# Kernel optimization log

Measured on AMD Instinct MI355X. Metric: run time of the kernel, lower is better.

The kernel has to match this reference:

```python
import jax, jax.numpy as jnp
import numpy as np

D_MODEL = 768
N_HEADS = 4
D_HEAD = D_MODEL // N_HEADS
EPS = 1e-3  # keras LayerNormalization default


def gelu_tanh(x):
    return 0.5 * x * (1.0 + jnp.tanh(np.sqrt(2.0 / np.pi) * (x + 0.044715 * x ** 3)))


def layer_norm(x, g, b):
    mu = jnp.mean(x, axis=-1, keepdims=True)
    var = jnp.mean(jnp.square(x - mu), axis=-1, keepdims=True)
    return (x - mu) * jax.lax.rsqrt(var + EPS) * g + b


def setup_inputs() -> dict:
    key = jax.random.key(0)
    ks = jax.random.split(key, 12)
    B, S = 8, 1024
    x = jax.random.normal(ks[0], (B, S, D_MODEL), dtype=jnp.float32)
    # causal mask: 1 on strictly-future positions (added as mask * -1e9)
    mask = jnp.triu(jnp.ones((S, S), dtype=jnp.float32), k=1)[None, None]
    s = 0.02
    params = {
        'W1': jax.random.normal(ks[1], (D_MODEL, 3 * D_MODEL)) * s,
        'b1': jnp.zeros((3 * D_MODEL,), jnp.float32),
        'W3': jax.random.normal(ks[2], (D_MODEL, D_MODEL)) * s,
        'b3': jnp.zeros((D_MODEL,), jnp.float32),
        'W2': jax.random.normal(ks[3], (D_MODEL, 4 * D_MODEL)) * s,
        'b2': jnp.zeros((4 * D_MODEL,), jnp.float32),
        'W4': jax.random.normal(ks[4], (4 * D_MODEL, D_MODEL)) * s,
        'b4': jnp.zeros((D_MODEL,), jnp.float32),
        'g1': jnp.ones((D_MODEL,), jnp.float32),
        'be1': jnp.zeros((D_MODEL,), jnp.float32),
        'g2': jnp.ones((D_MODEL,), jnp.float32),
        'be2': jnp.zeros((D_MODEL,), jnp.float32),
    }
    return {'x': x, 'mask': mask, **params}


def reference(x, mask, W1, b1, W3, b3, W2, b2, W4, b4, g1, be1, g2, be2):
    B, S, _ = x.shape
    xn = layer_norm(x, g1, be1)
    qkv = xn @ W1 + b1                                  # [B,S,3D]
    q, k, v = jnp.split(qkv, 3, axis=-1)
    def split_heads(t):
        return t.reshape(B, S, N_HEADS, D_HEAD).transpose(0, 2, 1, 3)  # [B,H,S,dh]
    q, k, v = map(split_heads, (q, k, v))
    present = jnp.stack([k, v], axis=1)                  # [B,2,H,S,dh]
    w = jnp.einsum('bhqd,bhkd->bhqk', q, k)
    # NOTE: source divides by rsqrt(d_head) => multiplies by sqrt(d_head) (faithful bug)
    w = w * jnp.sqrt(jnp.float32(D_HEAD))
    w = w + mask * -1e9
    w = jax.nn.softmax(w, axis=-1)
    attn = jnp.einsum('bhqk,bhkd->bhqd', w, v)           # [B,H,S,dh]
    attn = attn.transpose(0, 2, 1, 3).reshape(B, S, D_MODEL)
    x = attn @ W3 + b3 + x                               # residual 1
    xn2 = layer_norm(x, g2, be2)
    h = gelu_tanh(xn2 @ W2 + b2)                         # [B,S,4D]
    x = h @ W4 + b4 + x                                  # residual 2
    return x, present
```

## Files before the change

kernel.cpp:

```cpp
#include <hip/hip_runtime.h>
#include <hip/hip_bf16.h>
#include <cstdint>

#define D_MODEL 768
#define NH 4
#define DH 192
#define SEQ 1024
#define BATCH 8

typedef __bf16 bf16x8 __attribute__((ext_vector_type(8)));
typedef float floatx4 __attribute__((ext_vector_type(4)));

__device__ __forceinline__ float bf2f(ushort u) {
    union { uint32_t i; float f; } x; x.i = ((uint32_t)u) << 16; return x.f;
}
__device__ __forceinline__ ushort f2bf(float f) {
    union { float f; uint32_t i; } x; x.f = f;
    uint32_t i = x.i;
    uint32_t r = (i + 0x7FFFu + ((i >> 16) & 1u)) >> 16;
    return (ushort)r;
}

template <int SPLIT>
__global__ void ln_kernel(const float* __restrict__ x, const float* __restrict__ g,
                          const float* __restrict__ be,
                          ushort* __restrict__ y_hi, ushort* __restrict__ y_lo) {
    int row = blockIdx.x;
    int tid = threadIdx.x;
    const float* xr = x + (size_t)row * D_MODEL;
    float v[3];
    float s = 0.f, ss = 0.f;
#pragma unroll
    for (int i = 0; i < 3; i++) {
        float t = xr[tid + i * 256];
        v[i] = t; s += t; ss += t * t;
    }
#pragma unroll
    for (int off = 32; off > 0; off >>= 1) {
        s += __shfl_down(s, off);
        ss += __shfl_down(ss, off);
    }
    __shared__ float rs[4], rss[4];
    int wid = tid >> 6;
    if ((tid & 63) == 0) { rs[wid] = s; rss[wid] = ss; }
    __syncthreads();
    s = rs[0] + rs[1] + rs[2] + rs[3];
    ss = rss[0] + rss[1] + rss[2] + rss[3];
    float mu = s * (1.f / 768.f);
    float var = ss * (1.f / 768.f) - mu * mu;
    float rstd = rsqrtf(var + 1e-3f);
#pragma unroll
    for (int i = 0; i < 3; i++) {
        int d = tid + i * 256;
        float val = (v[i] - mu) * rstd * g[d] + be[d];
        ushort hi = f2bf(val);
        y_hi[(size_t)row * D_MODEL + d] = hi;
        if (SPLIT) y_lo[(size_t)row * D_MODEL + d] = f2bf(val - bf2f(hi));
    }
}

__global__ void transpose_kernel(const float* __restrict__ W, ushort* __restrict__ Wt,
                                 int K, int N) {
    __shared__ ushort tile[64][65];
    int nt = N >> 6;
    int bk = blockIdx.x / nt, bn = blockIdx.x % nt;
    int tid = threadIdx.x;
#pragma unroll
    for (int i = 0; i < 16; i++) {
        int lin = i * 256 + tid; int r = lin >> 6, c = lin & 63;
        tile[r][c] = f2bf(W[(size_t)(bk * 64 + r) * N + bn * 64 + c]);
    }
    __syncthreads();
#pragma unroll
    for (int i = 0; i < 16; i++) {
        int lin = i * 256 + tid; int r = lin >> 6, c = lin & 63;
        Wt[(size_t)(bn * 64 + r) * K + bk * 64 + c] = tile[c][r];
    }
}

__global__ void transpose_split_kernel(const float* __restrict__ W,
                                       ushort* __restrict__ Wt_hi, ushort* __restrict__ Wt_lo,
                                       int K, int N) {
    __shared__ ushort th[64][65];
    __shared__ ushort tl[64][65];
    int nt = N >> 6;
    int bk = blockIdx.x / nt, bn = blockIdx.x % nt;
    int tid = threadIdx.x;
#pragma unroll
    for (int i = 0; i < 16; i++) {
        int lin = i * 256 + tid; int r = lin >> 6, c = lin & 63;
        float v = W[(size_t)(bk * 64 + r) * N + bn * 64 + c];
        ushort hi = f2bf(v);
        th[r][c] = hi;
        tl[r][c] = f2bf(v - bf2f(hi));
    }
    __syncthreads();
#pragma unroll
    for (int i = 0; i < 16; i++) {
        int lin = i * 256 + tid; int r = lin >> 6, c = lin & 63;
        size_t o = (size_t)(bn * 64 + r) * K + bk * 64 + c;
        Wt_hi[o] = th[c][r];
        Wt_lo[o] = tl[c][r];
    }
}

__global__ void transpose_v_kernel(const float* __restrict__ qkv, ushort* __restrict__ Vtg) {
    __shared__ ushort tile[64][65];
    int bi = blockIdx.x;
    int dt = bi % 12;
    int st = (bi / 12) % 16;
    int b  = bi / 192;
    int tid = threadIdx.x;
#pragma unroll
    for (int i = 0; i < 16; i++) {
        int lin = i * 256 + tid; int r = lin >> 6, c = lin & 63;
        tile[r][c] = f2bf(qkv[(size_t)(b * 1024 + st * 64 + r) * 2304 + 1536 + dt * 64 + c]);
    }
    __syncthreads();
#pragma unroll
    for (int i = 0; i < 16; i++) {
        int lin = i * 256 + tid; int r = lin >> 6, c = lin & 63;
        Vtg[(size_t)(b * 768 + dt * 64 + r) * 1024 + st * 64 + c] = tile[c][r];
    }
}

__global__ __launch_bounds__(256, 2) void gemm_qkv_split(
    const ushort* __restrict__ Ah, const ushort* __restrict__ Al,
    const ushort* __restrict__ Bh, const ushort* __restrict__ Bl,
    const float* __restrict__ bias, float* __restrict__ Cout, int M, int N, int K) {
    __shared__ __align__(16) __bf16 sAh[128][48];
    __shared__ __align__(16) __bf16 sAl[128][48];
    __shared__ __align__(16) __bf16 sBh[128][48];
    __shared__ __align__(16) __bf16 sBl[128][48];
    int tid = threadIdx.x;
    int rowBase = blockIdx.y << 7;
    int colBase = blockIdx.x << 7;
    int wave = tid >> 6, lane = tid & 63;
    int wm = (wave & 1) << 6, wn = (wave >> 1) << 6;
    int lrow = lane & 15, lk = (lane >> 4) << 3;
    floatx4 acc[4][4] = {};

    int lr = tid >> 2;
    int lc = (tid & 3) << 3;
    size_t aoff = (size_t)(rowBase + lr) * K + lc;
    size_t boff = (size_t)(colBase + lr) * K + lc;

    for (int k0 = 0; k0 < K; k0 += 32) {
        uint4 ah0 = *(const uint4*)(Ah + aoff + k0);
        uint4 ah1 = *(const uint4*)(Ah + aoff + (size_t)64 * K + k0);
        uint4 al0 = *(const uint4*)(Al + aoff + k0);
        uint4 al1 = *(const uint4*)(Al + aoff + (size_t)64 * K + k0);
        uint4 bh0 = *(const uint4*)(Bh + boff + k0);
        uint4 bh1 = *(const uint4*)(Bh + boff + (size_t)64 * K + k0);
        uint4 bl0 = *(const uint4*)(Bl + boff + k0);
        uint4 bl1 = *(const uint4*)(Bl + boff + (size_t)64 * K + k0);
        *(uint4*)&sAh[lr][lc] = ah0;  *(uint4*)&sAh[lr + 64][lc] = ah1;
        *(uint4*)&sAl[lr][lc] = al0;  *(uint4*)&sAl[lr + 64][lc] = al1;
        *(uint4*)&sBh[lr][lc] = bh0;  *(uint4*)&sBh[lr + 64][lc] = bh1;
        *(uint4*)&sBl[lr][lc] = bl0;  *(uint4*)&sBl[lr + 64][lc] = bl1;
        __syncthreads();
        bf16x8 afh[4], afl[4], bvh[4], bvl[4];
#pragma unroll
        for (int i = 0; i < 4; i++) {
            afh[i] = *(const bf16x8*)&sAh[wm + i * 16 + lrow][lk];
            afl[i] = *(const bf16x8*)&sAl[wm + i * 16 + lrow][lk];
        }
#pragma unroll
        for (int jj = 0; jj < 4; jj++) {
            bvh[jj] = *(const bf16x8*)&sBh[wn + jj * 16 + lrow][lk];
            bvl[jj] = *(const bf16x8*)&sBl[wn + jj * 16 + lrow][lk];
        }
#pragma unroll
        for (int i = 0; i < 4; i++)
#pragma unroll
            for (int jj = 0; jj < 4; jj++) {
                acc[i][jj] = __builtin_amdgcn_mfma_f32_16x16x32_bf16(afh[i], bvh[jj], acc[i][jj], 0, 0, 0);
                acc[i][jj] = __builtin_amdgcn_mfma_f32_16x16x32_bf16(afh[i], bvl[jj], acc[i][jj], 0, 0, 0);
                acc[i][jj] = __builtin_amdgcn_mfma_f32_16x16x32_bf16(afl[i], bvh[jj], acc[i][jj], 0, 0, 0);
            }
        __syncthreads();
    }
    int cr = (lane >> 4) << 2;
    int cc = lane & 15;
#pragma unroll
    for (int jj = 0; jj < 4; jj++) {
        int col = colBase + wn + jj * 16 + cc;
        float bvs = bias[col];
#pragma unroll
        for (int i = 0; i < 4; i++) {
            int row0 = rowBase + wm + i * 16 + cr;
#pragma unroll
            for (int r = 0; r < 4; r++)
                Cout[(size_t)(row0 + r) * N + col] = acc[i][jj][r] + bvs;
        }
    }
}

template <int GELU, int RES, int OUTF32>
__global__ __launch_bounds__(256, 2) void gemm_bt(
    const ushort* __restrict__ A, const ushort* __restrict__ Bt,
    const float* __restrict__ bias, const float* __restrict__ resid,
    void* __restrict__ Cout, int M, int N, int K) {
    __shared__ __align__(16) __bf16 sA[128][48];
    __shared__ __align__(16) __bf16 sB[128][48];
    int tid = threadIdx.x;
    int rowBase = blockIdx.y << 7;
    int colBase = blockIdx.x << 7;
    int wave = tid >> 6, lane = tid & 63;
    int wm = (wave & 1) << 6, wn = (wave >> 1) << 6;
    int lrow = lane & 15, lk = (lane >> 4) << 3;
    floatx4 acc[4][4] = {};

    int lr = tid >> 2;
    int lc = (tid & 3) << 3;
    const ushort* Ab = A + (size_t)(rowBase + lr) * K + lc;
    const ushort* Bb = Bt + (size_t)(colBase + lr) * K + lc;

    for (int k0 = 0; k0 < K; k0 += 32) {
        uint4 a0 = *(const uint4*)(Ab + k0);
        uint4 a1 = *(const uint4*)(Ab + (size_t)64 * K + k0);
        uint4 b0 = *(const uint4*)(Bb + k0);
        uint4 b1 = *(const uint4*)(Bb + (size_t)64 * K + k0);
        *(uint4*)&sA[lr][lc] = a0;
        *(uint4*)&sA[lr + 64][lc] = a1;
        *(uint4*)&sB[lr][lc] = b0;
        *(uint4*)&sB[lr + 64][lc] = b1;
        __syncthreads();
        bf16x8 af[4], bv[4];
#pragma unroll
        for (int i = 0; i < 4; i++) af[i] = *(const bf16x8*)&sA[wm + i * 16 + lrow][lk];
#pragma unroll
        for (int jj = 0; jj < 4; jj++) bv[jj] = *(const bf16x8*)&sB[wn + jj * 16 + lrow][lk];
#pragma unroll
        for (int i = 0; i < 4; i++)
#pragma unroll
            for (int jj = 0; jj < 4; jj++)
                acc[i][jj] = __builtin_amdgcn_mfma_f32_16x16x32_bf16(af[i], bv[jj], acc[i][jj], 0, 0, 0);
        __syncthreads();
    }
    int cr = (lane >> 4) << 2;
    int cc = lane & 15;
#pragma unroll
    for (int jj = 0; jj < 4; jj++) {
        int col = colBase + wn + jj * 16 + cc;
        float bvs = bias[col];
#pragma unroll
        for (int i = 0; i < 4; i++) {
            int row0 = rowBase + wm + i * 16 + cr;
#pragma unroll
            for (int r = 0; r < 4; r++) {
                int row = row0 + r;
                float v = acc[i][jj][r] + bvs;
                if (GELU) {
                    float u = v;
                    v = 0.5f * u * (1.f + tanhf(0.7978845608028654f * (u + 0.044715f * u * u * u)));
                }
                if (RES) v += resid[(size_t)row * N + col];
                if (OUTF32) ((float*)Cout)[(size_t)row * N + col] = v;
                else ((ushort*)Cout)[(size_t)row * N + col] = f2bf(v);
            }
        }
    }
}

__global__ void split_kernel(const float* __restrict__ qkv, float* __restrict__ present,
                             ushort* __restrict__ Khg, ushort* __restrict__ Klg) {
    int tok = blockIdx.x;
    int tid = threadIdx.x;
    int b = tok >> 10, s = tok & 1023;
    const float* src = qkv + (size_t)tok * 2304 + 768;
#pragma unroll
    for (int i = 0; i < 6; i++) {
        int c = tid + i * 256;
        float v = src[c];
        int kv = (c >= 768) ? 1 : 0;
        int within = c - kv * 768;
        int h = within / DH;
        int d = within - h * DH;
        size_t idx = ((size_t)(((b * 2 + kv) * NH + h) * SEQ + s)) * DH + d;
        present[idx] = v;
        if (!kv) {
            ushort hi = f2bf(v);
            Khg[(size_t)tok * 768 + c] = hi;
            Klg[(size_t)tok * 768 + c] = f2bf(v - bf2f(hi));
        }
    }
}

__global__ __launch_bounds__(512, 2) void attn_flash(
    const float* __restrict__ qkv, const ushort* __restrict__ Khg,
    const ushort* __restrict__ Klg, const ushort* __restrict__ Vtg,
    ushort* __restrict__ attn2) {
    int bi = blockIdx.x;
    int j = bi & 7;
    int h = (bi >> 3) & 3;
    int b = bi >> 5;
    int tid = threadIdx.x;
    int wave = tid >> 6, lane = tid & 63;
    int l15 = lane & 15, quad = lane >> 4;
    int tile = (wave < 4) ? (15 - j) : j;
    int w16 = wave & 3;
    int s0 = tile << 6;
    int its = 2 * (15 - j) + 2;
    int myKt = (s0 + w16 * 16 + 15) >> 5;

    __shared__ __align__(16) __bf16 sKh[2][32][200];
    __shared__ __align__(16) __bf16 sKl[2][32][200];
    __shared__ __align__(16) __bf16 sVt[2][192][40];
    __shared__ __align__(16) ushort sP[8][16][40];

    const bool lo_half = (tid < 256);
    const int kr0 = tid / 24, ke0 = (tid % 24) * 8;
    const int c1 = lo_half ? (512 + tid) : (256 + tid);
    const int kr1 = c1 / 24, ke1 = (c1 % 24) * 8;
    const int vd0 = tid >> 2, ve0 = (tid & 3) * 8;
    const int vd1 = (512 + tid) >> 2, ve1 = ((512 + tid) & 3) * 8;

    const ushort* Khb = Khg + (size_t)(b * 1024) * 768 + h * 192;
    const ushort* Klb = Klg + (size_t)(b * 1024) * 768 + h * 192;
    const ushort* Vtb = Vtg + ((size_t)(b * 768) + h * 192) * 1024;
    const ushort* Bb = lo_half ? Khb : Klb;
    __bf16* pKB = lo_half ? &sKh[0][kr1][ke1] : &sKl[0][kr1][ke1];

    uint4 rA, rB, rC, rD, rE;

    rA = *(const uint4*)(Khb + (size_t)kr0 * 768 + ke0);
    rC = *(const uint4*)(Klb + (size_t)kr0 * 768 + ke0);
    rB = *(const uint4*)(Bb + (size_t)kr1 * 768 + ke1);
    rD = *(const uint4*)(Vtb + (size_t)vd0 * 1024 + ve0);
    if (lo_half) rE = *(const uint4*)(Vtb + (size_t)vd1 * 1024 + ve1);

    bf16x8 qh[6], ql[6];
    {
        int qrow = s0 + w16 * 16 + l15;
        const float* qp = qkv + (size_t)(b * SEQ + qrow) * 2304 + h * DH + quad * 8;
#pragma unroll
        for (int dt = 0; dt < 6; dt++) {
            float4 v0 = *(const float4*)(qp + dt * 32);
            float4 v1 = *(const float4*)(qp + dt * 32 + 4);
            float vv[8] = {v0.x, v0.y, v0.z, v0.w, v1.x, v1.y, v1.z, v1.w};
            bf16x8 hh, ll;
#pragma unroll
            for (int jj = 0; jj < 8; jj++) {
                float sv = vv[jj] * 13.856406460551018f;
                ushort hu = f2bf(sv);
                ((ushort*)&hh)[jj] = hu;
                ((ushort*)&ll)[jj] = f2bf(sv - bf2f(hu));
            }
            qh[dt] = hh; ql[dt] = ll;
        }
    }

    floatx4 O[12] = {};
    float m_run[4], l_run[4];
#pragma unroll
    for (int r = 0; r < 4; r++) { m_run[r] = -1e30f; l_run[r] = 0.f; }

    *(uint4*)&sKh[0][kr0][ke0] = rA;
    *(uint4*)&sKl[0][kr0][ke0] = rC;
    *(uint4*)(pKB) = rB;
    *(uint4*)&sVt[0][vd0][ve0] = rD;
    if (lo_half) *(uint4*)&sVt[0][vd1][ve1] = rE;
    __syncthreads();

    for (int kt = 0; kt < its; kt++) {
        int cur = kt & 1;
        bool pfetch = (kt + 1 < its);
        if (pfetch) {
            int koff = (kt + 1) * 32;
            rA = *(const uint4*)(Khb + (size_t)(koff + kr0) * 768 + ke0);
            rC = *(const uint4*)(Klb + (size_t)(koff + kr0) * 768 + ke0);
            rB = *(const uint4*)(Bb + (size_t)(koff + kr1) * 768 + ke1);
            rD = *(const uint4*)(Vtb + (size_t)vd0 * 1024 + koff + ve0);
            if (lo_half) rE = *(const uint4*)(Vtb + (size_t)vd1 * 1024 + koff + ve1);
        }
        if (kt <= myKt) {
            floatx4 S0 = {}, S1 = {};
#pragma unroll
            for (int dt = 0; dt < 6; dt++) {
                bf16x8 k0h = *(const bf16x8*)&sKh[cur][l15][dt * 32 + quad * 8];
                bf16x8 k0l = *(const bf16x8*)&sKl[cur][l15][dt * 32 + quad * 8];
                bf16x8 k1h = *(const bf16x8*)&sKh[cur][16 + l15][dt * 32 + quad * 8];
                bf16x8 k1l = *(const bf16x8*)&sKl[cur][16 + l15][dt * 32 + quad * 8];
                S0 = __builtin_amdgcn_mfma_f32_16x16x32_bf16(qh[dt], k0h, S0, 0, 0, 0);
                S0 = __builtin_amdgcn_mfma_f32_16x16x32_bf16(qh[dt], k0l, S0, 0, 0, 0);
                S0 = __builtin_amdgcn_mfma_f32_16x16x32_bf16(ql[dt], k0h, S0, 0, 0, 0);
                S1 = __builtin_amdgcn_mfma_f32_16x16x32_bf16(qh[dt], k1h, S1, 0, 0, 0);
                S1 = __builtin_amdgcn_mfma_f32_16x16x32_bf16(qh[dt], k1l, S1, 0, 0, 0);
                S1 = __builtin_amdgcn_mfma_f32_16x16x32_bf16(ql[dt], k1h, S1, 0, 0, 0);
            }
            int qg = s0 + w16 * 16 + quad * 4;
            int colb = kt * 32 + l15;
            float mt[4];
#pragma unroll
            for (int r = 0; r < 4; r++) {
                float a = (colb <= qg + r) ? S0[r] : -1e30f;
                float c = (colb + 16 <= qg + r) ? S1[r] : -1e30f;
                S0[r] = a; S1[r] = c;
                mt[r] = fmaxf(a, c);
            }
#pragma unroll
            for (int m = 1; m <= 8; m <<= 1)
#pragma unroll
                for (int r = 0; r < 4; r++) mt[r] = fmaxf(mt[r], __shfl_xor(mt[r], m));
            float alpha[4], rsum[4], P0[4], P1[4];
#pragma unroll
            for (int r = 0; r < 4; r++) {
                float mn = fmaxf(m_run[r], mt[r]);
                alpha[r] = __expf(m_run[r] - mn);
                m_run[r] = mn;
                P0[r] = __expf(S0[r] - mn);
                P1[r] = __expf(S1[r] - mn);
                rsum[r] = P0[r] + P1[r];
            }
#pragma unroll
            for (int m = 1; m <= 8; m <<= 1)
#pragma unroll
                for (int r = 0; r < 4; r++) rsum[r] += __shfl_xor(rsum[r], m);
#pragma unroll
            for (int r = 0; r < 4; r++) l_run[r] = l_run[r] * alpha[r] + rsum[r];
#pragma unroll
            for (int t = 0; t < 12; t++)
#pragma unroll
                for (int r = 0; r < 4; r++) O[t][r] *= alpha[r];
#pragma unroll
            for (int r = 0; r < 4; r++) {
                sP[wave][quad * 4 + r][l15]      = f2bf(P0[r]);
                sP[wave][quad * 4 + r][16 + l15] = f2bf(P1[r]);
            }
            bf16x8 pfrag = *(const bf16x8*)&sP[wave][l15][quad * 8];
#pragma unroll
            for (int t = 0; t < 12; t++) {
                bf16x8 vf = *(const bf16x8*)&sVt[cur][t * 16 + l15][quad * 8];
                O[t] = __builtin_amdgcn_mfma_f32_16x16x32_bf16(pfrag, vf, O[t], 0, 0, 0);
            }
        }
        if (pfetch) {
            int nb = cur ^ 1;
            *(uint4*)&sKh[nb][kr0][ke0] = rA;
            *(uint4*)&sKl[nb][kr0][ke0] = rC;
            *(uint4*)(pKB + nb * 6400) = rB;
            *(uint4*)&sVt[nb][vd0][ve0] = rD;
            if (lo_half) *(uint4*)&sVt[nb][vd1][ve1] = rE;
        }
        __syncthreads();
    }

    float inv[4];
#pragma unroll
    for (int r = 0; r < 4; r++) inv[r] = 1.f / l_run[r];
    int qrow = s0 + w16 * 16 + quad * 4;
#pragma unroll
    for (int t = 0; t < 12; t++)
#pragma unroll
        for (int r = 0; r < 4; r++)
            attn2[(size_t)(b * SEQ + qrow + r) * D_MODEL + h * DH + t * 16 + l15] =
                f2bf(O[t][r] * inv[r]);
}

extern "C" void kernel_launch(void* const* d_in, const int* in_sizes, int n_in,
                              void* d_out, int out_size, void* d_ws, size_t ws_size,
                              hipStream_t stream) {
    const float* x  = (const float*)d_in[0];
    const float* W1 = (const float*)d_in[2];
    const float* b1 = (const float*)d_in[3];
    const float* W3 = (const float*)d_in[4];
    const float* b3 = (const float*)d_in[5];
    const float* W2 = (const float*)d_in[6];
    const float* b2 = (const float*)d_in[7];
    const float* W4 = (const float*)d_in[8];
    const float* b4 = (const float*)d_in[9];
    const float* g1 = (const float*)d_in[10];
    const float* be1 = (const float*)d_in[11];
    const float* g2 = (const float*)d_in[12];
    const float* be2 = (const float*)d_in[13];

    char* ws = (char*)d_ws;
    ushort* W1t_hi = (ushort*)(ws + 0);
    ushort* W1t_lo = (ushort*)(ws + 3538944);
    ushort* W3t    = (ushort*)(ws + 7077888);
    ushort* W2t    = (ushort*)(ws + 8257536);
    ushort* W4t    = (ushort*)(ws + 12976128);
    ushort* xn_hi  = (ushort*)(ws + 17694720);
    ushort* attn2  = (ushort*)(ws + 17694720);
    ushort* xn_lo  = (ushort*)(ws + 30277632);
    ushort* Khg    = (ushort*)(ws + 30277632);
    ushort* xn2    = (ushort*)(ws + 30277632);
    float*  x1     = (float*)(ws + 42860544);
    ushort* Klg    = (ushort*)(ws + 42860544);
    ushort* Vtg    = (ushort*)(ws + 55443456);
    float*  qkvf   = (float*)(ws + 68026368);
    ushort* hbuf   = (ushort*)(ws + 68026368);

    float* out0 = (float*)d_out;
    float* present = out0 + 6291456;

    transpose_split_kernel<<<(768 / 64) * (2304 / 64), 256, 0, stream>>>(W1, W1t_hi, W1t_lo, 768, 2304);
    transpose_kernel<<<(768 / 64) * (768 / 64), 256, 0, stream>>>(W3, W3t, 768, 768);
    transpose_kernel<<<(768 / 64) * (3072 / 64), 256, 0, stream>>>(W2, W2t, 768, 3072);
    transpose_kernel<<<(3072 / 64) * (768 / 64), 256, 0, stream>>>(W4, W4t, 3072, 768);

    ln_kernel<1><<<8192, 256, 0, stream>>>(x, g1, be1, xn_hi, xn_lo);
    gemm_qkv_split<<<dim3(2304 / 128, 8192 / 128), 256, 0, stream>>>(
        xn_hi, xn_lo, W1t_hi, W1t_lo, b1, qkvf, 8192, 2304, 768);
    split_kernel<<<8192, 256, 0, stream>>>(qkvf, present, Khg, Klg);
    transpose_v_kernel<<<1536, 256, 0, stream>>>(qkvf, Vtg);
    attn_flash<<<BATCH * NH * 8, 512, 0, stream>>>(qkvf, Khg, Klg, Vtg, attn2);
    gemm_bt<0, 1, 1><<<dim3(768 / 128, 8192 / 128), 256, 0, stream>>>(
        attn2, W3t, b3, x, x1, 8192, 768, 768);
    ln_kernel<0><<<8192, 256, 0, stream>>>(x1, g2, be2, xn2, nullptr);
    gemm_bt<1, 0, 0><<<dim3(3072 / 128, 8192 / 128), 256, 0, stream>>>(
        xn2, W2t, b2, nullptr, hbuf, 8192, 3072, 768);
    gemm_bt<0, 1, 1><<<dim3(768 / 128, 8192 / 128), 256, 0, stream>>>(
        hbuf, W4t, b4, x1, out0, 8192, 768, 3072);
}
```

Before: 527.4 us.

## Fuse QKV split/transposes into GEMM epilogue; async double-buffered LDS loads in GEMMs

The QKV GEMM epilogue now writes Q as fp32, present K/V, the bf16 hi/lo K split and the transposed bf16 V directly. This removes the separate split_kernel and transpose_v_kernel and the fp32 qkv round trip through memory. Both GEMM kernels switch to global_load_lds direct-to-LDS loads with double buffering and an XOR swizzle to avoid bank conflicts, and gemm_bt raises its launch-bounds occupancy hint. The GELU tanh is replaced by the equivalent x*sigmoid form using __expf. The transposed V store from the epilogue is strided and uncoalesced, which may cost some of the saved bandwidth.

```diff
diff --git a/kernel.cpp b/kernel.cpp
--- a/kernel.cpp
+++ b/kernel.cpp
@@ -19,6 +19,12 @@
     uint32_t i = x.i;
     uint32_t r = (i + 0x7FFFu + ((i >> 16) & 1u)) >> 16;
     return (ushort)r;
+}
+
+__device__ __forceinline__ void gl_lds16(const void* g, void* l) {
+    __builtin_amdgcn_global_load_lds(
+        (const __attribute__((address_space(1))) uint32_t*)g,
+        (__attribute__((address_space(3))) uint32_t*)l, 16, 0, 0);
 }
 
 template <int SPLIT>
@@ -104,71 +110,61 @@
     }
 }
 
-__global__ void transpose_v_kernel(const float* __restrict__ qkv, ushort* __restrict__ Vtg) {
-    __shared__ ushort tile[64][65];
-    int bi = blockIdx.x;
-    int dt = bi % 12;
-    int st = (bi / 12) % 16;
-    int b  = bi / 192;
-    int tid = threadIdx.x;
-#pragma unroll
-    for (int i = 0; i < 16; i++) {
-        int lin = i * 256 + tid; int r = lin >> 6, c = lin & 63;
-        tile[r][c] = f2bf(qkv[(size_t)(b * 1024 + st * 64 + r) * 2304 + 1536 + dt * 64 + c]);
-    }
-    __syncthreads();
-#pragma unroll
-    for (int i = 0; i < 16; i++) {
-        int lin = i * 256 + tid; int r = lin >> 6, c = lin & 63;
-        Vtg[(size_t)(b * 768 + dt * 64 + r) * 1024 + st * 64 + c] = tile[c][r];
-    }
-}
-
 __global__ __launch_bounds__(256, 2) void gemm_qkv_split(
     const ushort* __restrict__ Ah, const ushort* __restrict__ Al,
     const ushort* __restrict__ Bh, const ushort* __restrict__ Bl,
-    const float* __restrict__ bias, float* __restrict__ Cout, int M, int N, int K) {
-    __shared__ __align__(16) __bf16 sAh[128][48];
-    __shared__ __align__(16) __bf16 sAl[128][48];
-    __shared__ __align__(16) __bf16 sBh[128][48];
-    __shared__ __align__(16) __bf16 sBl[128][48];
+    const float* __restrict__ bias,
+    float* __restrict__ Qf, float* __restrict__ present,
+    ushort* __restrict__ Khg, ushort* __restrict__ Klg, ushort* __restrict__ Vtg) {
+    const int K = 768;
+    __shared__ __align__(16) __bf16 sAh[2][128][32];
+    __shared__ __align__(16) __bf16 sAl[2][128][32];
+    __shared__ __align__(16) __bf16 sBh[2][128][32];
+    __shared__ __align__(16) __bf16 sBl[2][128][32];
     int tid = threadIdx.x;
     int rowBase = blockIdx.y << 7;
     int colBase = blockIdx.x << 7;
     int wave = tid >> 6, lane = tid & 63;
     int wm = (wave & 1) << 6, wn = (wave >> 1) << 6;
-    int lrow = lane & 15, lk = (lane >> 4) << 3;
+    int lrow = lane & 15, q = lane >> 4;
+    int lkswz = ((q ^ ((lrow >> 1) & 3)) << 3);
     floatx4 acc[4][4] = {};
 
-    int lr = tid >> 2;
-    int lc = (tid & 3) << 3;
-    size_t aoff = (size_t)(rowBase + lr) * K + lc;
-    size_t boff = (size_t)(colBase + lr) * K + lc;
-
-    for (int k0 = 0; k0 < K; k0 += 32) {
-        uint4 ah0 = *(const uint4*)(Ah + aoff + k0);
-        uint4 ah1 = *(const uint4*)(Ah + aoff + (size_t)64 * K + k0);
-        uint4 al0 = *(const uint4*)(Al + aoff + k0);
-        uint4 al1 = *(const uint4*)(Al + aoff + (size_t)64 * K + k0);
-        uint4 bh0 = *(const uint4*)(Bh + boff + k0);
-        uint4 bh1 = *(const uint4*)(Bh + boff + (size_t)64 * K + k0);
-        uint4 bl0 = *(const uint4*)(Bl + boff + k0);
-        uint4 bl1 = *(const uint4*)(Bl + boff + (size_t)64 * K + k0);
-        *(uint4*)&sAh[lr][lc] = ah0;  *(uint4*)&sAh[lr + 64][lc] = ah1;
-        *(uint4*)&sAl[lr][lc] = al0;  *(uint4*)&sAl[lr + 64][lc] = al1;
-        *(uint4*)&sBh[lr][lc] = bh0;  *(uint4*)&sBh[lr + 64][lc] = bh1;
-        *(uint4*)&sBl[lr][lc] = bl0;  *(uint4*)&sBl[lr + 64][lc] = bl1;
-        __syncthreads();
+    int srow = lane >> 2;
+    int schunk = (lane & 3) ^ ((lane >> 3) & 3);
+    const ushort* Ah0 = Ah + (size_t)(rowBase + wave * 32 + srow) * K + schunk * 8;
+    const ushort* Al0 = Al + (size_t)(rowBase + wave * 32 + srow) * K + schunk * 8;
+    const ushort* Bh0 = Bh + (size_t)(colBase + wave * 32 + srow) * K + schunk * 8;
+    const ushort* Bl0 = Bl + (size_t)(colBase + wave * 32 + srow) * K + schunk * 8;
+    const size_t r16 = (size_t)16 * K;
+    int wr = wave * 32;
+
+    gl_lds16(Ah0, &sAh[0][wr][0]);       gl_lds16(Ah0 + r16, &sAh[0][wr + 16][0]);
+    gl_lds16(Al0, &sAl[0][wr][0]);       gl_lds16(Al0 + r16, &sAl[0][wr + 16][0]);
+    gl_lds16(Bh0, &sBh[0][wr][0]);       gl_lds16(Bh0 + r16, &sBh[0][wr + 16][0]);
+    gl_lds16(Bl0, &sBl[0][wr][0]);       gl_lds16(Bl0 + r16, &sBl[0][wr + 16][0]);
+    __syncthreads();
+
+    const int nt = K >> 5;
+    for (int t = 0; t < nt; t++) {
+        int cur = t & 1, nb = cur ^ 1;
+        if (t + 1 < nt) {
+            int k0 = (t + 1) << 5;
+            gl_lds16(Ah0 + k0, &sAh[nb][wr][0]);  gl_lds16(Ah0 + r16 + k0, &sAh[nb][wr + 16][0]);
+            gl_lds16(Al0 + k0, &sAl[nb][wr][0]);  gl_lds16(Al0 + r16 + k0, &sAl[nb][wr + 16][0]);
+            gl_lds16(Bh0 + k0, &sBh[nb][wr][0]);  gl_lds16(Bh0 + r16 + k0, &sBh[nb][wr + 16][0]);
+            gl_lds16(Bl0 + k0, &sBl[nb][wr][0]);  gl_lds16(Bl0 + r16 + k0, &sBl[nb][wr + 16][0]);
+        }
         bf16x8 afh[4], afl[4], bvh[4], bvl[4];
 #pragma unroll
         for (int i = 0; i < 4; i++) {
-            afh[i] = *(const bf16x8*)&sAh[wm + i * 16 + lrow][lk];
-            afl[i] = *(const bf16x8*)&sAl[wm + i * 16 + lrow][lk];
+            afh[i] = *(const bf16x8*)&sAh[cur][wm + i * 16 + lrow][lkswz];
+            afl[i] = *(const bf16x8*)&sAl[cur][wm + i * 16 + lrow][lkswz];
         }
 #pragma unroll
         for (int jj = 0; jj < 4; jj++) {
-            bvh[jj] = *(const bf16x8*)&sBh[wn + jj * 16 + lrow][lk];
-            bvl[jj] = *(const bf16x8*)&sBl[wn + jj * 16 + lrow][lk];
+            bvh[jj] = *(const bf16x8*)&sBh[cur][wn + jj * 16 + lrow][lkswz];
+            bvl[jj] = *(const bf16x8*)&sBl[cur][wn + jj * 16 + lrow][lkswz];
         }
 #pragma unroll
         for (int i = 0; i < 4; i++)
@@ -180,57 +176,97 @@
             }
         __syncthreads();
     }
+
     int cr = (lane >> 4) << 2;
     int cc = lane & 15;
 #pragma unroll
     for (int jj = 0; jj < 4; jj++) {
         int col = colBase + wn + jj * 16 + cc;
         float bvs = bias[col];
-#pragma unroll
-        for (int i = 0; i < 4; i++) {
-            int row0 = rowBase + wm + i * 16 + cr;
-#pragma unroll
-            for (int r = 0; r < 4; r++)
-                Cout[(size_t)(row0 + r) * N + col] = acc[i][jj][r] + bvs;
+        if (colBase < 768) {
+#pragma unroll
+            for (int i = 0; i < 4; i++) {
+                int row0 = rowBase + wm + i * 16 + cr;
+#pragma unroll
+                for (int r = 0; r < 4; r++)
+                    Qf[(size_t)(row0 + r) * 768 + col] = acc[i][jj][r] + bvs;
+            }
+        } else if (colBase < 1536) {
+            int kc = col - 768;
+            int h = kc / DH, d = kc - h * DH;
+#pragma unroll
+            for (int i = 0; i < 4; i++) {
+                int row0 = rowBase + wm + i * 16 + cr;
+#pragma unroll
+                for (int r = 0; r < 4; r++) {
+                    int row = row0 + r;
+                    int b = row >> 10, s = row & 1023;
+                    float v = acc[i][jj][r] + bvs;
+                    present[((size_t)((b * 2) * NH + h) * SEQ + s) * DH + d] = v;
+                    ushort hi = f2bf(v);
+                    Khg[(size_t)row * 768 + kc] = hi;
+                    Klg[(size_t)row * 768 + kc] = f2bf(v - bf2f(hi));
+                }
+            }
+        } else {
+            int vc = col - 1536;
+            int h = vc / DH, d = vc - h * DH;
+#pragma unroll
+            for (int i = 0; i < 4; i++) {
+                int row0 = rowBase + wm + i * 16 + cr;
+#pragma unroll
+                for (int r = 0; r < 4; r++) {
+                    int row = row0 + r;
+                    int b = row >> 10, s = row & 1023;
+                    float v = acc[i][jj][r] + bvs;
+                    present[((size_t)((b * 2 + 1) * NH + h) * SEQ + s) * DH + d] = v;
+                    Vtg[((size_t)b * 768 + vc) * 1024 + s] = f2bf(v);
+                }
+            }
         }
     }
 }
 
 template <int GELU, int RES, int OUTF32>
-__global__ __launch_bounds__(256, 2) void gemm_bt(
+__global__ __launch_bounds__(256, 4) void gemm_bt(
     const ushort* __restrict__ A, const ushort* __restrict__ Bt,
     const float* __restrict__ bias, const float* __restrict__ resid,
     void* __restrict__ Cout, int M, int N, int K) {
-    __shared__ __align__(16) __bf16 sA[128][48];
-    __shared__ __align__(16) __bf16 sB[128][48];
+    __shared__ __align__(16) __bf16 sA[2][128][32];
+    __shared__ __align__(16) __bf16 sB[2][128][32];
     int tid = threadIdx.x;
     int rowBase = blockIdx.y << 7;
     int colBase = blockIdx.x << 7;
     int wave = tid >> 6, lane = tid & 63;
     int wm = (wave & 1) << 6, wn = (wave >> 1) << 6;
-    int lrow = lane & 15, lk = (lane >> 4) << 3;
+    int lrow = lane & 15, q = lane >> 4;
+    int lkswz = ((q ^ ((lrow >> 1) & 3)) << 3);
     floatx4 acc[4][4] = {};
 
-    int lr = tid >> 2;
-    int lc = (tid & 3) << 3;
-    const ushort* Ab = A + (size_t)(rowBase + lr) * K + lc;
-    const ushort* Bb = Bt + (size_t)(colBase + lr) * K + lc;
-
-    for (int k0 = 0; k0 < K; k0 += 32) {
-        uint4 a0 = *(const uint4*)(Ab + k0);
-        uint4 a1 = *(const uint4*)(Ab + (size_t)64 * K + k0);
-        uint4 b0 = *(const uint4*)(Bb + k0);
-        uint4 b1 = *(const uint4*)(Bb + (size_t)64 * K + k0);
-        *(uint4*)&sA[lr][lc] = a0;
-        *(uint4*)&sA[lr + 64][lc] = a1;
-        *(uint4*)&sB[lr][lc] = b0;
-        *(uint4*)&sB[lr + 64][lc] = b1;
-        __syncthreads();
+    int srow = lane >> 2;
+    int schunk = (lane & 3) ^ ((lane >> 3) & 3);
+    const ushort* Ag0 = A + (size_t)(rowBase + wave * 32 + srow) * K + schunk * 8;
+    const ushort* Bg0 = Bt + (size_t)(colBase + wave * 32 + srow) * K + schunk * 8;
+    const size_t r16 = (size_t)16 * K;
+    int wr = wave * 32;
+
+    gl_lds16(Ag0, &sA[0][wr][0]);  gl_lds16(Ag0 + r16, &sA[0][wr + 16][0]);
+    gl_lds16(Bg0, &sB[0][wr][0]);  gl_lds16(Bg0 + r16, &sB[0][wr + 16][0]);
+    __syncthreads();
+
+    int nt = K >> 5;
+    for (int t = 0; t < nt; t++) {
+        int cur = t & 1, nb = cur ^ 1;
+        if (t + 1 < nt) {
+            int k0 = (t + 1) << 5;
+            gl_lds16(Ag0 + k0, &sA[nb][wr][0]);  gl_lds16(Ag0 + r16 + k0, &sA[nb][wr + 16][0]);
+            gl_lds16(Bg0 + k0, &sB[nb][wr][0]);  gl_lds16(Bg0 + r16 + k0, &sB[nb][wr + 16][0]);
+        }
         bf16x8 af[4], bv[4];
 #pragma unroll
-        for (int i = 0; i < 4; i++) af[i] = *(const bf16x8*)&sA[wm + i * 16 + lrow][lk];
-#pragma unroll
-        for (int jj = 0; jj < 4; jj++) bv[jj] = *(const bf16x8*)&sB[wn + jj * 16 + lrow][lk];
+        for (int i = 0; i < 4; i++) af[i] = *(const bf16x8*)&sA[cur][wm + i * 16 + lrow][lkswz];
+#pragma unroll
+        for (int jj = 0; jj < 4; jj++) bv[jj] = *(const bf16x8*)&sB[cur][wn + jj * 16 + lrow][lkswz];
 #pragma unroll
         for (int i = 0; i < 4; i++)
 #pragma unroll
@@ -253,7 +289,8 @@
                 float v = acc[i][jj][r] + bvs;
                 if (GELU) {
                     float u = v;
-                    v = 0.5f * u * (1.f + tanhf(0.7978845608028654f * (u + 0.044715f * u * u * u)));
+                    float z2 = -1.5957691216057308f * (u + 0.044715f * u * u * u);
+                    v = u / (1.f + __expf(z2));
                 }
                 if (RES) v += resid[(size_t)row * N + col];
                 if (OUTF32) ((float*)Cout)[(size_t)row * N + col] = v;
@@ -263,32 +300,8 @@
     }
 }
 
-__global__ void split_kernel(const float* __restrict__ qkv, float* __restrict__ present,
-                             ushort* __restrict__ Khg, ushort* __restrict__ Klg) {
-    int tok = blockIdx.x;
-    int tid = threadIdx.x;
-    int b = tok >> 10, s = tok & 1023;
-    const float* src = qkv + (size_t)tok * 2304 + 768;
-#pragma unroll
-    for (int i = 0; i < 6; i++) {
-        int c = tid + i * 256;
-        float v = src[c];
-        int kv = (c >= 768) ? 1 : 0;
-        int within = c - kv * 768;
-        int h = within / DH;
-        int d = within - h * DH;
-        size_t idx = ((size_t)(((b * 2 + kv) * NH + h) * SEQ + s)) * DH + d;
-        present[idx] = v;
-        if (!kv) {
-            ushort hi = f2bf(v);
-            Khg[(size_t)tok * 768 + c] = hi;
-            Klg[(size_t)tok * 768 + c] = f2bf(v - bf2f(hi));
-        }
-    }
-}
-
 __global__ __launch_bounds__(512, 2) void attn_flash(
-    const float* __restrict__ qkv, const ushort* __restrict__ Khg,
+    const float* __restrict__ Qf, const ushort* __restrict__ Khg,
     const ushort* __restrict__ Klg, const ushort* __restrict__ Vtg,
     ushort* __restrict__ attn2) {
     int bi = blockIdx.x;
@@ -333,7 +346,7 @@
     bf16x8 qh[6], ql[6];
     {
         int qrow = s0 + w16 * 16 + l15;
-        const float* qp = qkv + (size_t)(b * SEQ + qrow) * 2304 + h * DH + quad * 8;
+        const float* qp = Qf + (size_t)(b * SEQ + qrow) * 768 + h * DH + quad * 8;
 #pragma unroll
         for (int dt = 0; dt < 6; dt++) {
             float4 v0 = *(const float4*)(qp + dt * 32);
@@ -484,13 +497,13 @@
     ushort* xn_hi  = (ushort*)(ws + 17694720);
     ushort* attn2  = (ushort*)(ws + 17694720);
     ushort* xn_lo  = (ushort*)(ws + 30277632);
-    ushort* Khg    = (ushort*)(ws + 30277632);
     ushort* xn2    = (ushort*)(ws + 30277632);
-    float*  x1     = (float*)(ws + 42860544);
-    ushort* Klg    = (ushort*)(ws + 42860544);
-    ushort* Vtg    = (ushort*)(ws + 55443456);
-    float*  qkvf   = (float*)(ws + 68026368);
-    ushort* hbuf   = (ushort*)(ws + 68026368);
+    float*  Qf     = (float*)(ws + 42860544);
+    ushort* hbuf   = (ushort*)(ws + 42860544);
+    ushort* Khg    = (ushort*)(ws + 68026368);
+    ushort* Klg    = (ushort*)(ws + 80609280);
+    ushort* Vtg    = (ushort*)(ws + 93192192);
+    float*  x1     = (float*)(ws + 105775104);
 
     float* out0 = (float*)d_out;
     float* present = out0 + 6291456;
@@ -502,10 +515,8 @@
 
     ln_kernel<1><<<8192, 256, 0, stream>>>(x, g1, be1, xn_hi, xn_lo);
     gemm_qkv_split<<<dim3(2304 / 128, 8192 / 128), 256, 0, stream>>>(
-        xn_hi, xn_lo, W1t_hi, W1t_lo, b1, qkvf, 8192, 2304, 768);
-    split_kernel<<<8192, 256, 0, stream>>>(qkvf, present, Khg, Klg);
-    transpose_v_kernel<<<1536, 256, 0, stream>>>(qkvf, Vtg);
-    attn_flash<<<BATCH * NH * 8, 512, 0, stream>>>(qkvf, Khg, Klg, Vtg, attn2);
+        xn_hi, xn_lo, W1t_hi, W1t_lo, b1, Qf, present, Khg, Klg, Vtg);
+    attn_flash<<<BATCH * NH * 8, 512, 0, stream>>>(Qf, Khg, Klg, Vtg, attn2);
     gemm_bt<0, 1, 1><<<dim3(768 / 128, 8192 / 128), 256, 0, stream>>>(
         attn2, W3t, b3, x, x1, 8192, 768, 768);
     ln_kernel<0><<<8192, 256, 0, stream>>>(x1, g2, be2, xn2, nullptr);
```

Result: faster. 513.1 us (-2.7%).
